# Optimization experiments

Measured on AMD Instinct MI355X. Metric: run time of the kernel, lower is better.

## Reference

```python
import jax, jax.numpy as jnp
import numpy as np

IN_DIM = 256
QK_DIM = IN_DIM // 8


def setup_inputs() -> dict:
    key = jax.random.key(0)
    ks = jax.random.split(key, 6)
    x = jax.random.normal(ks[0], (8, IN_DIM, 64, 64), dtype=jnp.float32)
    # 1x1 conv == per-pixel linear; store weights as [out, in]
    q_w = jax.random.normal(ks[1], (QK_DIM, IN_DIM), dtype=jnp.float32) * (1.0 / np.sqrt(IN_DIM))
    q_b = jax.random.normal(ks[2], (QK_DIM,), dtype=jnp.float32) * 0.01
    v_w = jax.random.normal(ks[3], (IN_DIM, IN_DIM), dtype=jnp.float32) * (1.0 / np.sqrt(IN_DIM))
    v_b = jax.random.normal(ks[4], (IN_DIM,), dtype=jnp.float32) * 0.01
    gamma = jnp.zeros((1,), dtype=jnp.float32) + 0.5  # nonzero so attention branch contributes
    return {"x": x, "q_w": q_w, "q_b": q_b, "v_w": v_w, "v_b": v_b, "gamma": gamma}


def reference(x, q_w, q_b, v_w, v_b, gamma):
    b, c, h, w = x.shape
    n = h * w
    xf = x.reshape(b, c, n)                                    # [b, c, n]
    # NOTE: original forward uses q_conv for BOTH q and k (k_conv unused)
    q = jnp.einsum('oc,bcn->bon', q_w, xf) + q_b[None, :, None]  # [b, d, n]
    proj_q = jnp.transpose(q, (0, 2, 1))                       # [b, n, d]
    energy = jnp.einsum('bid,bdj->bij', proj_q, q)             # [b, n, n]
    attention = jax.nn.softmax(energy, axis=-1)
    v = jnp.einsum('oc,bcn->bon', v_w, xf) + v_b[None, :, None]  # [b, c, n]
    # out[b,c,i] = sum_j v[b,c,j] * attention[b,i,j]
    out = jnp.einsum('bcj,bij->bci', v, attention)
    out = out.reshape(b, c, h, w)
    return gamma * out + x
```

## Files before the change

### kernel.cpp

```cpp
#include <hip/hip_runtime.h>

#define B_   8
#define C_   256
#define D_   32
#define N_   4096
#define FMX  64.0f

typedef __attribute__((ext_vector_type(8))) short bf8_t;
typedef __attribute__((ext_vector_type(4))) float f4_t;

__device__ __forceinline__ unsigned short f2bf(float f) {
    unsigned int u = __builtin_bit_cast(unsigned int, f);
    u += 0x7FFFu + ((u >> 16) & 1u);
    return (unsigned short)(u >> 16);
}
__device__ __forceinline__ float bf2f(unsigned short h) {
    unsigned int u = ((unsigned int)h) << 16;
    return __builtin_bit_cast(float, u);
}

__global__ __launch_bounds__(256) void wprep_kernel(
    const float* __restrict__ qw, const float* __restrict__ vw,
    unsigned short* __restrict__ wqh, unsigned short* __restrict__ wql,
    unsigned short* __restrict__ wvb)
{
    const int gid = blockIdx.x * 256 + threadIdx.x;
    const int nthr = gridDim.x * 256;
    for (int idx = gid; idx < 16384; idx += nthr) {
        float4 v = ((const float4*)vw)[idx];
        uint2 u;
        u.x = f2bf(v.x) | ((unsigned)f2bf(v.y) << 16);
        u.y = f2bf(v.z) | ((unsigned)f2bf(v.w) << 16);
        ((uint2*)wvb)[idx] = u;
    }
    for (int idx = gid; idx < 2048; idx += nthr) {
        float4 v = ((const float4*)qw)[idx];
        unsigned short h0 = f2bf(v.x), h1 = f2bf(v.y), h2 = f2bf(v.z), h3 = f2bf(v.w);
        uint2 uh, ul;
        uh.x = h0 | ((unsigned)h1 << 16);  uh.y = h2 | ((unsigned)h3 << 16);
        ul.x = f2bf(v.x - bf2f(h0)) | ((unsigned)f2bf(v.y - bf2f(h1)) << 16);
        ul.y = f2bf(v.z - bf2f(h2)) | ((unsigned)f2bf(v.w - bf2f(h3)) << 16);
        ((uint2*)wqh)[idx] = uh;
        ((uint2*)wql)[idx] = ul;
    }
}

__global__ __launch_bounds__(256, 2) void proj_kernel(
    const float* __restrict__ x, const unsigned short* __restrict__ wqh,
    const unsigned short* __restrict__ wql, const unsigned short* __restrict__ wvb,
    const float* __restrict__ qb, const float* __restrict__ vb,
    unsigned short* __restrict__ qh, unsigned short* __restrict__ ql,
    unsigned short* __restrict__ vT)
{
    __shared__ __align__(16) unsigned short S[32768];

    const int t    = threadIdx.x;
    const int lane = t & 63;
    const int w    = t >> 6;
    const int q4   = lane >> 4;
    const int l15  = lane & 15;
    const int b    = blockIdx.x >> 6;
    const int i0   = (blockIdx.x & 63) * 64;

    const float* xb = x + (size_t)b * C_ * N_;
    #pragma unroll
    for (int k = 0; k < 16; ++k) {
        int f4i = k * 256 + t;
        int c = f4i >> 4, col = (f4i & 15) << 2;
        float4 v = *(const float4*)(xb + (size_t)c * N_ + i0 + col);
        int chi = c >> 3, clo = c & 7;
        float vv[4] = {v.x, v.y, v.z, v.w};
        #pragma unroll
        for (int j = 0; j < 4; ++j) {
            unsigned short h = f2bf(vv[j]);
            unsigned short l = f2bf(vv[j] - bf2f(h));
            S[chi * 512 + (col + j) * 8 + clo]         = h;
            S[16384 + chi * 512 + (col + j) * 8 + clo] = l;
        }
    }
    __syncthreads();

    f4_t acc[4][4];
    #pragma unroll
    for (int mt = 0; mt < 4; ++mt)
        #pragma unroll
        for (int nt = 0; nt < 4; ++nt) acc[mt][nt] = (f4_t)0.0f;
    f4_t qacc[2];
    qacc[0] = (f4_t)0.0f; qacc[1] = (f4_t)0.0f;

    #pragma unroll
    for (int kk = 0; kk < 8; ++kk) {
        bf8_t Bh[4];
        #pragma unroll
        for (int nt = 0; nt < 4; ++nt)
            Bh[nt] = *(const bf8_t*)&S[(kk * 4 + q4) * 512 + (nt * 16 + l15) * 8];
        bf8_t Bl = *(const bf8_t*)&S[16384 + (kk * 4 + q4) * 512 + (w * 16 + l15) * 8];

        bf8_t Av[4];
        #pragma unroll
        for (int mt = 0; mt < 4; ++mt)
            Av[mt] = *(const bf8_t*)&wvb[(w * 64 + mt * 16 + l15) * 256 + kk * 32 + q4 * 8];
        bf8_t Aqh[2], Aql[2];
        #pragma unroll
        for (int mq = 0; mq < 2; ++mq) {
            Aqh[mq] = *(const bf8_t*)&wqh[(mq * 16 + l15) * 256 + kk * 32 + q4 * 8];
            Aql[mq] = *(const bf8_t*)&wql[(mq * 16 + l15) * 256 + kk * 32 + q4 * 8];
        }

        #pragma unroll
        for (int mt = 0; mt < 4; ++mt)
            #pragma unroll
            for (int nt = 0; nt < 4; ++nt)
                acc[mt][nt] = __builtin_amdgcn_mfma_f32_16x16x32_bf16(
                    Av[mt], Bh[nt], acc[mt][nt], 0, 0, 0);
        #pragma unroll
        for (int mq = 0; mq < 2; ++mq) {
            qacc[mq] = __builtin_amdgcn_mfma_f32_16x16x32_bf16(Aqh[mq], Bh[w], qacc[mq], 0, 0, 0);
            qacc[mq] = __builtin_amdgcn_mfma_f32_16x16x32_bf16(Aql[mq], Bh[w], qacc[mq], 0, 0, 0);
            qacc[mq] = __builtin_amdgcn_mfma_f32_16x16x32_bf16(Aqh[mq], Bl,    qacc[mq], 0, 0, 0);
        }
    }

    {
        const int iq = i0 + w * 16 + l15;
        #pragma unroll
        for (int mq = 0; mq < 2; ++mq) {
            float4 qb4 = *(const float4*)(qb + mq * 16 + q4 * 4);
            float qv[4] = {qacc[mq][0] + qb4.x, qacc[mq][1] + qb4.y,
                           qacc[mq][2] + qb4.z, qacc[mq][3] + qb4.w};
            unsigned short hr[4], lr[4];
            #pragma unroll
            for (int r = 0; r < 4; ++r) {
                hr[r] = f2bf(qv[r]);
                lr[r] = f2bf(qv[r] - bf2f(hr[r]));
            }
            uint2 uh, ul;
            uh.x = hr[0] | ((unsigned)hr[1] << 16); uh.y = hr[2] | ((unsigned)hr[3] << 16);
            ul.x = lr[0] | ((unsigned)lr[1] << 16); ul.y = lr[2] | ((unsigned)lr[3] << 16);
            size_t qoff = ((size_t)b * N_ + iq) * D_ + mq * 16 + q4 * 4;
            *(uint2*)(qh + qoff) = uh;
            *(uint2*)(ql + qoff) = ul;
        }
    }

    __syncthreads();
    #pragma unroll
    for (int mt = 0; mt < 4; ++mt) {
        float4 vb4 = *(const float4*)(vb + w * 64 + mt * 16 + q4 * 4);
        float bias[4] = {vb4.x, vb4.y, vb4.z, vb4.w};
        #pragma unroll
        for (int nt = 0; nt < 4; ++nt)
            #pragma unroll
            for (int r = 0; r < 4; ++r)
                S[(w * 64 + mt * 16 + q4 * 4 + r) * 64 + nt * 16 + l15] =
                    f2bf(acc[mt][nt][r] + bias[r]);
    }
    __syncthreads();
    #pragma unroll
    for (int k2 = 0; k2 < 8; ++k2) {
        int id = k2 * 256 + t;
        int oc = id >> 3, seg = id & 7;
        uint4 dat = *(const uint4*)&S[oc * 64 + seg * 8];
        *(uint4*)(vT + ((size_t)b * C_ + oc) * N_ + i0 + seg * 8) = dat;
    }
}

__global__ __launch_bounds__(256, 2) void attn_kernel(
    const unsigned short* __restrict__ qh, const unsigned short* __restrict__ ql,
    const unsigned short* __restrict__ vT, const float* __restrict__ x,
    const float* __restrict__ gamma_p, float* __restrict__ out)
{
    __shared__ __align__(16) unsigned short Vs[8 * 257 * 8];
    __shared__ __align__(16) unsigned short Pb[8 * 64 * 8];
    __shared__ __align__(16) float rowl[64];

    float* T = (float*)Vs;

    const int t    = threadIdx.x;
    const int lane = t & 63;
    const int w    = t >> 6;
    const int q4   = lane >> 4;
    const int l15  = lane & 15;
    const int b    = blockIdx.x >> 6;
    const int i0   = (blockIdx.x & 63) * 64;

    const unsigned short* qhb = qh + (size_t)b * N_ * D_;
    const unsigned short* qlb = ql + (size_t)b * N_ * D_;
    const unsigned short* vTb = vT + (size_t)b * C_ * N_;

    bf8_t Ah[4], Al[4];
    #pragma unroll
    for (int mt = 0; mt < 4; ++mt) {
        size_t off = (size_t)(i0 + mt * 16 + l15) * D_ + q4 * 8;
        Ah[mt] = *(const bf8_t*)(qhb + off);
        Al[mt] = *(const bf8_t*)(qlb + off);
    }

    f4_t acc[4][4];
    #pragma unroll
    for (int mt = 0; mt < 4; ++mt)
        #pragma unroll
        for (int nt = 0; nt < 4; ++nt) acc[mt][nt] = (f4_t)0.0f;

    f4_t lacc[4];
    #pragma unroll
    for (int mt = 0; mt < 4; ++mt) lacc[mt] = (f4_t)0.0f;
    bf8_t onesb;
    #pragma unroll
    for (int e = 0; e < 8; ++e) onesb[e] = (short)0x3F80;

    for (int jt = 0; jt < N_ / 64; ++jt) {
        const int j0 = jt * 64;

        size_t koff = (size_t)(j0 + w * 16 + l15) * D_ + q4 * 8;
        bf8_t Bh = *(const bf8_t*)(qhb + koff);
        bf8_t Bl = *(const bf8_t*)(qlb + koff);

        __syncthreads();

        #pragma unroll
        for (int r = 0; r < 8; ++r) {
            int idx = r * 256 + t;
            int c = idx >> 3, part = idx & 7;
            uint4 d = *(const uint4*)(vTb + (size_t)c * N_ + j0 + part * 8);
            *(uint4*)(&Vs[(part * 257 + c) * 8]) = d;
        }

        f4_t s[4];
        #pragma unroll
        for (int mt = 0; mt < 4; ++mt) {
            f4_t a = (f4_t)0.0f;
            a = __builtin_amdgcn_mfma_f32_16x16x32_bf16(Ah[mt], Bh, a, 0, 0, 0);
            a = __builtin_amdgcn_mfma_f32_16x16x32_bf16(Ah[mt], Bl, a, 0, 0, 0);
            a = __builtin_amdgcn_mfma_f32_16x16x32_bf16(Al[mt], Bh, a, 0, 0, 0);
            s[mt] = a;
        }

        const int jl = w * 16 + l15;
        const int pprt = jl >> 3, jlo = jl & 7;
        #pragma unroll
        for (int mt = 0; mt < 4; ++mt)
            #pragma unroll
            for (int r = 0; r < 4; ++r) {
                float p = __expf(s[mt][r] - FMX);
                Pb[(pprt * 64 + mt * 16 + q4 * 4 + r) * 8 + jlo] = f2bf(p);
            }

        __syncthreads();

        #pragma unroll
        for (int kk = 0; kk < 2; ++kk) {
            bf8_t Af[4], Bf[4];
            #pragma unroll
            for (int mt = 0; mt < 4; ++mt)
                Af[mt] = *(const bf8_t*)(&Pb[((kk * 4 + q4) * 64 + mt * 16 + l15) * 8]);
            #pragma unroll
            for (int nt = 0; nt < 4; ++nt)
                Bf[nt] = *(const bf8_t*)(&Vs[((kk * 4 + q4) * 257 + w * 64 + nt * 16 + l15) * 8]);
            #pragma unroll
            for (int mt = 0; mt < 4; ++mt)
                #pragma unroll
                for (int nt = 0; nt < 4; ++nt)
                    acc[mt][nt] = __builtin_amdgcn_mfma_f32_16x16x32_bf16(
                        Af[mt], Bf[nt], acc[mt][nt], 0, 0, 0);
            if (w == 3) {
                #pragma unroll
                for (int mt = 0; mt < 4; ++mt)
                    lacc[mt] = __builtin_amdgcn_mfma_f32_16x16x32_bf16(
                        Af[mt], onesb, lacc[mt], 0, 0, 0);
            }
        }
    }

    __syncthreads();
    if (w == 3 && l15 == 0) {
        #pragma unroll
        for (int mt = 0; mt < 4; ++mt)
            #pragma unroll
            for (int r = 0; r < 4; ++r)
                rowl[mt * 16 + q4 * 4 + r] = lacc[mt][r];
    }
    __syncthreads();

    const float g = gamma_p[0];
    for (int mt = 0; mt < 4; ++mt) {
        float4 rl = *(float4*)(&rowl[mt * 16 + q4 * 4]);
        float inv[4] = { g / rl.x, g / rl.y, g / rl.z, g / rl.w };
        #pragma unroll
        for (int nt = 0; nt < 4; ++nt)
            #pragma unroll
            for (int r = 0; r < 4; ++r)
                T[(w * 64 + nt * 16 + l15) * 17 + q4 * 4 + r] = acc[mt][nt][r] * inv[r];
        __syncthreads();
        #pragma unroll
        for (int pass = 0; pass < 4; ++pass) {
            int c  = pass * 64 + (t >> 2);
            int ii = (t & 3) * 4;
            float4 o;
            o.x = T[c * 17 + ii];     o.y = T[c * 17 + ii + 1];
            o.z = T[c * 17 + ii + 2]; o.w = T[c * 17 + ii + 3];
            size_t goff = ((size_t)b * C_ + c) * N_ + i0 + mt * 16 + ii;
            float4 xv = *(const float4*)(x + goff);
            o.x += xv.x; o.y += xv.y; o.z += xv.z; o.w += xv.w;
            *(float4*)(out + goff) = o;
        }
        __syncthreads();
    }
}

extern "C" void kernel_launch(void* const* d_in, const int* in_sizes, int n_in,
                              void* d_out, int out_size, void* d_ws, size_t ws_size,
                              hipStream_t stream)
{
    const float* x     = (const float*)d_in[0];
    const float* q_w   = (const float*)d_in[1];
    const float* q_b   = (const float*)d_in[2];
    const float* v_w   = (const float*)d_in[3];
    const float* v_b   = (const float*)d_in[4];
    const float* gamma = (const float*)d_in[5];
    float* out = (float*)d_out;

    unsigned short* ws16 = (unsigned short*)d_ws;
    unsigned short* qhp = ws16;
    unsigned short* qlp = ws16 + 1048576;
    unsigned short* vTp = ws16 + 2097152;
    unsigned short* wvb = ws16 + 10485760;
    unsigned short* wqh = wvb + 65536;
    unsigned short* wql = wqh + 8192;

    wprep_kernel<<<24, 256, 0, stream>>>(q_w, v_w, wqh, wql, wvb);
    proj_kernel<<<B_ * (N_ / 64), 256, 0, stream>>>(x, wqh, wql, wvb, q_b, v_b,
                                                    qhp, qlp, vTp);
    attn_kernel<<<B_ * (N_ / 64), 256, 0, stream>>>(qhp, qlp, vTp, x, gamma, out);
}
```

Before: 259.8 us.

## Store V and weights in MFMA fragment layout, read V directly from global

Weights and the V projection are written in the MFMA operand fragment order, so the attention kernel loads V fragments straight from global memory into registers. This removes the per-tile LDS staging of V and one barrier per iteration. P is double-buffered in padded LDS, and the row-sum MFMA is spread across all four waves instead of done only by wave 3. The projection also drops the low-order bf16 term of x for q, which halves the x staging work but slightly lowers q precision.

```diff
diff --git a/kernel.cpp b/kernel.cpp
--- a/kernel.cpp
+++ b/kernel.cpp
@@ -5,6 +5,7 @@
 #define D_   32
 #define N_   4096
 #define FMX  64.0f
+#define PBS  520
 
 typedef __attribute__((ext_vector_type(8))) short bf8_t;
 typedef __attribute__((ext_vector_type(4))) float f4_t;
@@ -18,41 +19,52 @@
     unsigned int u = ((unsigned int)h) << 16;
     return __builtin_bit_cast(float, u);
 }
+__device__ __forceinline__ uint4 pack8(const unsigned short* h) {
+    uint4 u;
+    u.x = h[0] | ((unsigned)h[1] << 16); u.y = h[2] | ((unsigned)h[3] << 16);
+    u.z = h[4] | ((unsigned)h[5] << 16); u.w = h[6] | ((unsigned)h[7] << 16);
+    return u;
+}
 
 __global__ __launch_bounds__(256) void wprep_kernel(
     const float* __restrict__ qw, const float* __restrict__ vw,
-    unsigned short* __restrict__ wqh, unsigned short* __restrict__ wql,
-    unsigned short* __restrict__ wvb)
+    unsigned short* __restrict__ wqFh, unsigned short* __restrict__ wqFl,
+    unsigned short* __restrict__ wvF)
 {
-    const int gid = blockIdx.x * 256 + threadIdx.x;
-    const int nthr = gridDim.x * 256;
-    for (int idx = gid; idx < 16384; idx += nthr) {
-        float4 v = ((const float4*)vw)[idx];
-        uint2 u;
-        u.x = f2bf(v.x) | ((unsigned)f2bf(v.y) << 16);
-        u.y = f2bf(v.z) | ((unsigned)f2bf(v.w) << 16);
-        ((uint2*)wvb)[idx] = u;
-    }
-    for (int idx = gid; idx < 2048; idx += nthr) {
-        float4 v = ((const float4*)qw)[idx];
-        unsigned short h0 = f2bf(v.x), h1 = f2bf(v.y), h2 = f2bf(v.z), h3 = f2bf(v.w);
-        uint2 uh, ul;
-        uh.x = h0 | ((unsigned)h1 << 16);  uh.y = h2 | ((unsigned)h3 << 16);
-        ul.x = f2bf(v.x - bf2f(h0)) | ((unsigned)f2bf(v.y - bf2f(h1)) << 16);
-        ul.y = f2bf(v.z - bf2f(h2)) | ((unsigned)f2bf(v.w - bf2f(h3)) << 16);
-        ((uint2*)wqh)[idx] = uh;
-        ((uint2*)wql)[idx] = ul;
+    const int tid = blockIdx.x * 256 + threadIdx.x;
+    if (tid < 8192) {
+        const int k = tid;
+        const int rowblk = k >> 9, kk = (k >> 6) & 7, lane = k & 63;
+        const int oc = rowblk * 16 + (lane & 15), c0 = kk * 32 + (lane >> 4) * 8;
+        const float* src = vw + oc * 256 + c0;
+        unsigned short h[8];
+        #pragma unroll
+        for (int e = 0; e < 8; ++e) h[e] = f2bf(src[e]);
+        *(uint4*)(wvF + (size_t)k * 8) = pack8(h);
+    } else if (tid < 9216) {
+        const int k = tid - 8192;
+        const int rowblk = k >> 9, kk = (k >> 6) & 7, lane = k & 63;
+        const int oc = rowblk * 16 + (lane & 15), c0 = kk * 32 + (lane >> 4) * 8;
+        const float* src = qw + oc * 256 + c0;
+        unsigned short h[8], l[8];
+        #pragma unroll
+        for (int e = 0; e < 8; ++e) {
+            h[e] = f2bf(src[e]);
+            l[e] = f2bf(src[e] - bf2f(h[e]));
+        }
+        *(uint4*)(wqFh + (size_t)k * 8) = pack8(h);
+        *(uint4*)(wqFl + (size_t)k * 8) = pack8(l);
     }
 }
 
 __global__ __launch_bounds__(256, 2) void proj_kernel(
-    const float* __restrict__ x, const unsigned short* __restrict__ wqh,
-    const unsigned short* __restrict__ wql, const unsigned short* __restrict__ wvb,
+    const float* __restrict__ x, const unsigned short* __restrict__ wqFh,
+    const unsigned short* __restrict__ wqFl, const unsigned short* __restrict__ wvF,
     const float* __restrict__ qb, const float* __restrict__ vb,
     unsigned short* __restrict__ qh, unsigned short* __restrict__ ql,
-    unsigned short* __restrict__ vT)
+    unsigned short* __restrict__ vF)
 {
-    __shared__ __align__(16) unsigned short S[32768];
+    __shared__ __align__(16) unsigned short S[18432];
 
     const int t    = threadIdx.x;
     const int lane = t & 63;
@@ -60,23 +72,20 @@
     const int q4   = lane >> 4;
     const int l15  = lane & 15;
     const int b    = blockIdx.x >> 6;
-    const int i0   = (blockIdx.x & 63) * 64;
-
-    const float* xb = x + (size_t)b * C_ * N_;
-    #pragma unroll
-    for (int k = 0; k < 16; ++k) {
-        int f4i = k * 256 + t;
-        int c = f4i >> 4, col = (f4i & 15) << 2;
-        float4 v = *(const float4*)(xb + (size_t)c * N_ + i0 + col);
-        int chi = c >> 3, clo = c & 7;
-        float vv[4] = {v.x, v.y, v.z, v.w};
-        #pragma unroll
-        for (int j = 0; j < 4; ++j) {
-            unsigned short h = f2bf(vv[j]);
-            unsigned short l = f2bf(vv[j] - bf2f(h));
-            S[chi * 512 + (col + j) * 8 + clo]         = h;
-            S[16384 + chi * 512 + (col + j) * 8 + clo] = l;
-        }
+    const int tile = blockIdx.x & 63;
+    const int i0   = tile * 64;
+
+    const float* xb = x + (size_t)b * C_ * N_ + i0 + lane;
+    #pragma unroll
+    for (int cc = 0; cc < 8; ++cc) {
+        const int chi = w * 8 + cc;
+        float v[8];
+        #pragma unroll
+        for (int e = 0; e < 8; ++e) v[e] = xb[(size_t)(chi * 8 + e) * N_];
+        unsigned short h[8];
+        #pragma unroll
+        for (int e = 0; e < 8; ++e) h[e] = f2bf(v[e]);
+        *(uint4*)&S[(chi * 64 + lane) * 8] = pack8(h);
     }
     __syncthreads();
 
@@ -93,18 +102,16 @@
         bf8_t Bh[4];
         #pragma unroll
         for (int nt = 0; nt < 4; ++nt)
-            Bh[nt] = *(const bf8_t*)&S[(kk * 4 + q4) * 512 + (nt * 16 + l15) * 8];
-        bf8_t Bl = *(const bf8_t*)&S[16384 + (kk * 4 + q4) * 512 + (w * 16 + l15) * 8];
-
+            Bh[nt] = *(const bf8_t*)&S[((kk * 4 + q4) * 64 + nt * 16 + l15) * 8];
         bf8_t Av[4];
         #pragma unroll
         for (int mt = 0; mt < 4; ++mt)
-            Av[mt] = *(const bf8_t*)&wvb[(w * 64 + mt * 16 + l15) * 256 + kk * 32 + q4 * 8];
+            Av[mt] = *(const bf8_t*)&wvF[(size_t)(((w * 4 + mt) * 8 + kk) * 64 + lane) * 8];
         bf8_t Aqh[2], Aql[2];
         #pragma unroll
         for (int mq = 0; mq < 2; ++mq) {
-            Aqh[mq] = *(const bf8_t*)&wqh[(mq * 16 + l15) * 256 + kk * 32 + q4 * 8];
-            Aql[mq] = *(const bf8_t*)&wql[(mq * 16 + l15) * 256 + kk * 32 + q4 * 8];
+            Aqh[mq] = *(const bf8_t*)&wqFh[(size_t)((mq * 8 + kk) * 64 + lane) * 8];
+            Aql[mq] = *(const bf8_t*)&wqFl[(size_t)((mq * 8 + kk) * 64 + lane) * 8];
         }
 
         #pragma unroll
@@ -117,7 +124,6 @@
         for (int mq = 0; mq < 2; ++mq) {
             qacc[mq] = __builtin_amdgcn_mfma_f32_16x16x32_bf16(Aqh[mq], Bh[w], qacc[mq], 0, 0, 0);
             qacc[mq] = __builtin_amdgcn_mfma_f32_16x16x32_bf16(Aql[mq], Bh[w], qacc[mq], 0, 0, 0);
-            qacc[mq] = __builtin_amdgcn_mfma_f32_16x16x32_bf16(Aqh[mq], Bl,    qacc[mq], 0, 0, 0);
         }
     }
 
@@ -152,7 +158,7 @@
         for (int nt = 0; nt < 4; ++nt)
             #pragma unroll
             for (int r = 0; r < 4; ++r)
-                S[(w * 64 + mt * 16 + q4 * 4 + r) * 64 + nt * 16 + l15] =
+                S[(w * 64 + mt * 16 + q4 * 4 + r) * 72 + nt * 16 + l15] =
                     f2bf(acc[mt][nt][r] + bias[r]);
     }
     __syncthreads();
@@ -160,21 +166,18 @@
     for (int k2 = 0; k2 < 8; ++k2) {
         int id = k2 * 256 + t;
         int oc = id >> 3, seg = id & 7;
-        uint4 dat = *(const uint4*)&S[oc * 64 + seg * 8];
-        *(uint4*)(vT + ((size_t)b * C_ + oc) * N_ + i0 + seg * 8) = dat;
+        uint4 dat = *(const uint4*)&S[oc * 72 + seg * 8];
+        *(uint4*)(vF + ((((size_t)b * 64 + tile) * 8 + seg) * 256 + oc) * 8) = dat;
     }
 }
 
 __global__ __launch_bounds__(256, 2) void attn_kernel(
     const unsigned short* __restrict__ qh, const unsigned short* __restrict__ ql,
-    const unsigned short* __restrict__ vT, const float* __restrict__ x,
+    const unsigned short* __restrict__ vF, const float* __restrict__ x,
     const float* __restrict__ gamma_p, float* __restrict__ out)
 {
-    __shared__ __align__(16) unsigned short Vs[8 * 257 * 8];
-    __shared__ __align__(16) unsigned short Pb[8 * 64 * 8];
+    __shared__ __align__(16) unsigned short LS[8704];
     __shared__ __align__(16) float rowl[64];
-
-    float* T = (float*)Vs;
 
     const int t    = threadIdx.x;
     const int lane = t & 63;
@@ -186,7 +189,7 @@
 
     const unsigned short* qhb = qh + (size_t)b * N_ * D_;
     const unsigned short* qlb = ql + (size_t)b * N_ * D_;
-    const unsigned short* vTb = vT + (size_t)b * C_ * N_;
+    const unsigned short* vFb = vF + (size_t)b * 64 * 8 * 256 * 8;
 
     bf8_t Ah[4], Al[4];
     #pragma unroll
@@ -201,30 +204,23 @@
     for (int mt = 0; mt < 4; ++mt)
         #pragma unroll
         for (int nt = 0; nt < 4; ++nt) acc[mt][nt] = (f4_t)0.0f;
-
-    f4_t lacc[4];
-    #pragma unroll
-    for (int mt = 0; mt < 4; ++mt) lacc[mt] = (f4_t)0.0f;
+    f4_t lacc = (f4_t)0.0f;
     bf8_t onesb;
     #pragma unroll
     for (int e = 0; e < 8; ++e) onesb[e] = (short)0x3F80;
 
     for (int jt = 0; jt < N_ / 64; ++jt) {
-        const int j0 = jt * 64;
-
-        size_t koff = (size_t)(j0 + w * 16 + l15) * D_ + q4 * 8;
+        size_t koff = (size_t)(jt * 64 + w * 16 + l15) * D_ + q4 * 8;
         bf8_t Bh = *(const bf8_t*)(qhb + koff);
         bf8_t Bl = *(const bf8_t*)(qlb + koff);
 
-        __syncthreads();
-
-        #pragma unroll
-        for (int r = 0; r < 8; ++r) {
-            int idx = r * 256 + t;
-            int c = idx >> 3, part = idx & 7;
-            uint4 d = *(const uint4*)(vTb + (size_t)c * N_ + j0 + part * 8);
-            *(uint4*)(&Vs[(part * 257 + c) * 8]) = d;
-        }
+        bf8_t Bf[2][4];
+        #pragma unroll
+        for (int kk = 0; kk < 2; ++kk)
+            #pragma unroll
+            for (int nt = 0; nt < 4; ++nt)
+                Bf[kk][nt] = *(const bf8_t*)&vFb[
+                    (((size_t)jt * 8 + kk * 4 + q4) * 256 + w * 64 + nt * 16 + l15) * 8];
 
         f4_t s[4];
         #pragma unroll
@@ -236,6 +232,7 @@
             s[mt] = a;
         }
 
+        unsigned short* Pb = LS + (jt & 1) * 4160;
         const int jl = w * 16 + l15;
         const int pprt = jl >> 3, jlo = jl & 7;
         #pragma unroll
@@ -243,46 +240,35 @@
             #pragma unroll
             for (int r = 0; r < 4; ++r) {
                 float p = __expf(s[mt][r] - FMX);
-                Pb[(pprt * 64 + mt * 16 + q4 * 4 + r) * 8 + jlo] = f2bf(p);
+                Pb[pprt * PBS + (mt * 16 + q4 * 4 + r) * 8 + jlo] = f2bf(p);
             }
 
         __syncthreads();
 
         #pragma unroll
         for (int kk = 0; kk < 2; ++kk) {
-            bf8_t Af[4], Bf[4];
+            bf8_t Af[4];
             #pragma unroll
             for (int mt = 0; mt < 4; ++mt)
-                Af[mt] = *(const bf8_t*)(&Pb[((kk * 4 + q4) * 64 + mt * 16 + l15) * 8]);
-            #pragma unroll
-            for (int nt = 0; nt < 4; ++nt)
-                Bf[nt] = *(const bf8_t*)(&Vs[((kk * 4 + q4) * 257 + w * 64 + nt * 16 + l15) * 8]);
+                Af[mt] = *(const bf8_t*)&Pb[(kk * 4 + q4) * PBS + (mt * 16 + l15) * 8];
             #pragma unroll
             for (int mt = 0; mt < 4; ++mt)
                 #pragma unroll
                 for (int nt = 0; nt < 4; ++nt)
                     acc[mt][nt] = __builtin_amdgcn_mfma_f32_16x16x32_bf16(
-                        Af[mt], Bf[nt], acc[mt][nt], 0, 0, 0);
-            if (w == 3) {
-                #pragma unroll
-                for (int mt = 0; mt < 4; ++mt)
-                    lacc[mt] = __builtin_amdgcn_mfma_f32_16x16x32_bf16(
-                        Af[mt], onesb, lacc[mt], 0, 0, 0);
-            }
-        }
-    }
-
+                        Af[mt], Bf[kk][nt], acc[mt][nt], 0, 0, 0);
+            lacc = __builtin_amdgcn_mfma_f32_16x16x32_bf16(Af[w], onesb, lacc, 0, 0, 0);
+        }
+    }
+
+    if (l15 == 0) {
+        #pragma unroll
+        for (int r = 0; r < 4; ++r) rowl[w * 16 + q4 * 4 + r] = lacc[r];
+    }
     __syncthreads();
-    if (w == 3 && l15 == 0) {
-        #pragma unroll
-        for (int mt = 0; mt < 4; ++mt)
-            #pragma unroll
-            for (int r = 0; r < 4; ++r)
-                rowl[mt * 16 + q4 * 4 + r] = lacc[mt][r];
-    }
-    __syncthreads();
 
     const float g = gamma_p[0];
+    float* T = (float*)LS;
     for (int mt = 0; mt < 4; ++mt) {
         float4 rl = *(float4*)(&rowl[mt * 16 + q4 * 4]);
         float inv[4] = { g / rl.x, g / rl.y, g / rl.z, g / rl.w };
@@ -321,15 +307,15 @@
     float* out = (float*)d_out;
 
     unsigned short* ws16 = (unsigned short*)d_ws;
-    unsigned short* qhp = ws16;
-    unsigned short* qlp = ws16 + 1048576;
-    unsigned short* vTp = ws16 + 2097152;
-    unsigned short* wvb = ws16 + 10485760;
-    unsigned short* wqh = wvb + 65536;
-    unsigned short* wql = wqh + 8192;
-
-    wprep_kernel<<<24, 256, 0, stream>>>(q_w, v_w, wqh, wql, wvb);
-    proj_kernel<<<B_ * (N_ / 64), 256, 0, stream>>>(x, wqh, wql, wvb, q_b, v_b,
-                                                    qhp, qlp, vTp);
-    attn_kernel<<<B_ * (N_ / 64), 256, 0, stream>>>(qhp, qlp, vTp, x, gamma, out);
-}
+    unsigned short* qhp  = ws16;
+    unsigned short* qlp  = ws16 + 1048576;
+    unsigned short* vFp  = ws16 + 2097152;
+    unsigned short* wvF  = ws16 + 10485760;
+    unsigned short* wqFh = wvF + 65536;
+    unsigned short* wqFl = wqFh + 8192;
+
+    wprep_kernel<<<36, 256, 0, stream>>>(q_w, v_w, wqFh, wqFl, wvF);
+    proj_kernel<<<B_ * (N_ / 64), 256, 0, stream>>>(x, wqFh, wqFl, wvF, q_b, v_b,
+                                                    qhp, qlp, vFp);
+    attn_kernel<<<B_ * (N_ / 64), 256, 0, stream>>>(qhp, qlp, vFp, x, gamma, out);
+}
```

Result: slower. 370.5 us (+42.6%).
